# Kernel optimization log

Measured on AMD Instinct MI355X. Metric: run time of the kernel, lower is better.

## Reference

```python
import jax, jax.numpy as jnp
import numpy as np

B, L, D, H, FF = 4, 1024, 768, 12, 3072
DK = D // H
P = 32          # num_postags
MAXD = 256      # max relative distance


def _ln(x, g, b, eps):
    mu = jnp.mean(x, axis=-1, keepdims=True)
    var = jnp.mean(jnp.square(x - mu), axis=-1, keepdims=True)
    return (x - mu) * jax.lax.rsqrt(var + eps) * g + b


def setup_inputs() -> dict:
    key = jax.random.key(0)
    ks = jax.random.split(key, 16)
    s = 0.02
    return {
        "x": jax.random.normal(ks[0], (B, L, D), jnp.float32),
        "postag_ids": jax.random.randint(ks[1], (B, L), 0, P),
        "lex_mask": jax.random.normal(ks[2], (B, L), jnp.float32),
        "ln1_g": jnp.ones((D,), jnp.float32),
        "ln1_b": jnp.zeros((D,), jnp.float32),
        "Wq": jax.random.normal(ks[3], (D, D), jnp.float32) * s,
        "bq": jnp.zeros((D,), jnp.float32),
        "Wk": jax.random.normal(ks[4], (D, D), jnp.float32) * s,
        "bk": jnp.zeros((D,), jnp.float32),
        "Wv": jax.random.normal(ks[5], (D, D), jnp.float32) * s,
        "bv": jnp.zeros((D,), jnp.float32),
        "Wo": jax.random.normal(ks[6], (D, D), jnp.float32) * s,
        "bo": jnp.zeros((D,), jnp.float32),
        "rel_emb": jax.random.normal(ks[7], (2 * MAXD + 1, H), jnp.float32) * s,
        "postag_table": jax.random.normal(ks[8], (P * P, H), jnp.float32) * s,
        "ln2_g": jnp.ones((D,), jnp.float32),
        "ln2_b": jnp.zeros((D,), jnp.float32),
        "W1": jax.random.normal(ks[9], (D, FF), jnp.float32) * s,
        "b1": jnp.zeros((FF,), jnp.float32),
        "W2": jax.random.normal(ks[10], (FF, D), jnp.float32) * s,
        "b2": jnp.zeros((D,), jnp.float32),
    }


def reference(x, postag_ids, lex_mask, ln1_g, ln1_b, Wq, bq, Wk, bk, Wv, bv,
              Wo, bo, rel_emb, postag_table, ln2_g, ln2_b, W1, b1, W2, b2):
    # ---- pre-LN self-attention with rel-pos + postag + lex additive biases ----
    q_in = _ln(x, ln1_g, ln1_b, 1e-6)
    Q = (q_in @ Wq + bq).reshape(B, L, H, DK).transpose(0, 2, 1, 3)  # [B,H,L,dk]
    K = (q_in @ Wk + bk).reshape(B, L, H, DK).transpose(0, 2, 1, 3)
    V = (q_in @ Wv + bv).reshape(B, L, H, DK).transpose(0, 2, 1, 3)

    logits = jnp.einsum("bhld,bhsd->bhls", Q, K) / jnp.sqrt(jnp.float32(DK))

    # relative position bias: [H, L, L]
    idx = jnp.arange(L)
    rel = idx[None, :] - idx[:, None]
    clipped = jnp.clip(rel, -MAXD, MAXD) + MAXD
    pos_bias = rel_emb[clipped].transpose(2, 0, 1)  # [H,L,L]

    # postag pair bias: [B, H, L, L]
    pair = postag_ids[:, :, None] * P + postag_ids[:, None, :]  # [B,L,L]
    pt_bias = postag_table[pair].transpose(0, 3, 1, 2)  # [B,H,L,L]

    logits = logits + pos_bias[None] + pt_bias + lex_mask[:, None, None, :]

    attn = jax.nn.softmax(logits, axis=-1)
    out = jnp.einsum("bhls,bhsd->bhld", attn, V)
    out = out.transpose(0, 2, 1, 3).reshape(B, L, D)
    out = out @ Wo + bo + x  # residual

    # ---- FeedForward (pre-LN, exact GELU) ----
    h = _ln(out, ln2_g, ln2_b, 1e-5)
    h = jax.nn.gelu(h @ W1 + b1, approximate=False)
    return out + h @ W2 + b2
```

## Files before the change

### kernel.cpp

```cpp
#include <hip/hip_runtime.h>
#include <hip/hip_bf16.h>
#include <math.h>

typedef __hip_bfloat16 bf16;
typedef __attribute__((ext_vector_type(8))) short short8;
typedef __attribute__((ext_vector_type(4))) float f32x4;

#define BB 4
#define LL 1024
#define DD 768
#define HH 12
#define DK 64
#define FF_ 3072
#define PP 32
#define MAXD 256

__device__ __forceinline__ void async_load16(const void* g, void* l) {
    __builtin_amdgcn_global_load_lds(
        (const __attribute__((address_space(1))) unsigned int*)g,
        (__attribute__((address_space(3))) unsigned int*)l, 16, 0, 0);
}

__global__ __launch_bounds__(256) void ln_kernel(const float* __restrict__ x,
                                                 const float* __restrict__ g,
                                                 const float* __restrict__ b,
                                                 float eps,
                                                 bf16* __restrict__ y) {
    const int row = blockIdx.x;
    const int tid = threadIdx.x;
    const float* xr = x + (size_t)row * DD;

    float v[3];
    float s = 0.f, ss = 0.f;
#pragma unroll
    for (int i = 0; i < 3; ++i) {
        float t = xr[tid + i * 256];
        v[i] = t;
        s += t;
        ss += t * t;
    }
    __shared__ float rs[256], rss[256];
    rs[tid] = s; rss[tid] = ss;
    __syncthreads();
    for (int off = 128; off; off >>= 1) {
        if (tid < off) { rs[tid] += rs[tid + off]; rss[tid] += rss[tid + off]; }
        __syncthreads();
    }
    const float mean = rs[0] * (1.f / DD);
    const float var  = rss[0] * (1.f / DD) - mean * mean;
    const float inv  = rsqrtf(var + eps);
#pragma unroll
    for (int i = 0; i < 3; ++i) {
        int c = tid + i * 256;
        float o = (v[i] - mean) * inv * g[c] + b[c];
        y[(size_t)row * DD + c] = __float2bfloat16(o);
    }
}

__global__ __launch_bounds__(256) void ln_sum_kernel(const float* __restrict__ Wp,
                                                     const float* __restrict__ x,
                                                     const float* __restrict__ bo,
                                                     const float* __restrict__ g,
                                                     const float* __restrict__ b,
                                                     float eps,
                                                     float* __restrict__ out1,
                                                     bf16* __restrict__ h2) {
    const int row = blockIdx.x;
    const int tid = threadIdx.x;
    const size_t base = (size_t)row * DD;
    const size_t half = (size_t)BB * LL * DD;

    float v[3];
    float s = 0.f, ss = 0.f;
#pragma unroll
    for (int i = 0; i < 3; ++i) {
        int c = tid + i * 256;
        float t = Wp[base + c] + Wp[half + base + c] + bo[c] + x[base + c];
        out1[base + c] = t;
        v[i] = t;
        s += t;
        ss += t * t;
    }
    __shared__ float rs[256], rss[256];
    rs[tid] = s; rss[tid] = ss;
    __syncthreads();
    for (int off = 128; off; off >>= 1) {
        if (tid < off) { rs[tid] += rs[tid + off]; rss[tid] += rss[tid + off]; }
        __syncthreads();
    }
    const float mean = rs[0] * (1.f / DD);
    const float var  = rss[0] * (1.f / DD) - mean * mean;
    const float inv  = rsqrtf(var + eps);
#pragma unroll
    for (int i = 0; i < 3; ++i) {
        int c = tid + i * 256;
        float o = (v[i] - mean) * inv * g[c] + b[c];
        h2[base + c] = __float2bfloat16(o);
    }
}

__global__ __launch_bounds__(256) void ff2_reduce(const float* __restrict__ Fp,
                                                  const float* __restrict__ out1,
                                                  const float* __restrict__ b2,
                                                  float* __restrict__ dout) {
    const size_t half = (size_t)BB * LL * DD;
    const size_t i4 = (size_t)blockIdx.x * 256 + threadIdx.x;
    const size_t i = i4 * 4;
    const int c = (int)(i % DD);
    float4 p0 = *(const float4*)(Fp + i);
    float4 p1 = *(const float4*)(Fp + half + i);
    float4 r  = *(const float4*)(out1 + i);
    float4 o;
    o.x = p0.x + p1.x + r.x + b2[c];
    o.y = p0.y + p1.y + r.y + b2[c + 1];
    o.z = p0.z + p1.z + r.z + b2[c + 2];
    o.w = p0.w + p1.w + r.w + b2[c + 3];
    *(float4*)(dout + i) = o;
}

__global__ __launch_bounds__(256) void prep_weights(
        const float* __restrict__ Wq, const float* __restrict__ Wk,
        const float* __restrict__ Wv, const float* __restrict__ Wo,
        const float* __restrict__ W1, const float* __restrict__ W2,
        const float* __restrict__ bq, const float* __restrict__ bk,
        const float* __restrict__ bv,
        bf16* __restrict__ WtQKV, bf16* __restrict__ WtO,
        bf16* __restrict__ Wt1, bf16* __restrict__ Wt2,
        float* __restrict__ bqkv) {
    const int bid = blockIdx.x;
    if (bid >= 6912) {
        int i = (bid - 6912) * 256 + threadIdx.x;
        if (i < 2304) {
            float v = (i < 768) ? bq[i] : (i < 1536) ? bk[i - 768] : bv[i - 1536];
            bqkv[i] = v;
        }
        return;
    }
    const float* W; bf16* Wt; int K, N, tile;
    if (bid < 576)       { W = Wq; Wt = WtQKV;                      K = DD;  N = DD;  tile = bid; }
    else if (bid < 1152) { W = Wk; Wt = WtQKV + (size_t)768 * DD;   K = DD;  N = DD;  tile = bid - 576; }
    else if (bid < 1728) { W = Wv; Wt = WtQKV + (size_t)1536 * DD;  K = DD;  N = DD;  tile = bid - 1152; }
    else if (bid < 2304) { W = Wo; Wt = WtO;                        K = DD;  N = DD;  tile = bid - 1728; }
    else if (bid < 4608) { W = W1; Wt = Wt1;                        K = DD;  N = FF_; tile = bid - 2304; }
    else                 { W = W2; Wt = Wt2;                        K = FF_; N = DD;  tile = bid - 4608; }
    const int ntn = N / 32;
    const int n0 = (tile % ntn) * 32, k0 = (tile / ntn) * 32;

    __shared__ float tilebuf[32][33];
    const int tx = threadIdx.x & 31, ty = threadIdx.x >> 5;
#pragma unroll
    for (int i = 0; i < 4; ++i) {
        int k = ty + i * 8;
        tilebuf[k][tx] = W[(size_t)(k0 + k) * N + n0 + tx];
    }
    __syncthreads();
#pragma unroll
    for (int i = 0; i < 4; ++i) {
        int n = ty + i * 8;
        Wt[(size_t)(n0 + n) * K + k0 + tx] = __float2bfloat16(tilebuf[tx][n]);
    }
}

template <int RES, bool GELU, bool SPLIT_QKV, int KSPLIT, typename OutT>
__global__ __launch_bounds__(256) void mfma_gemm_bt(const bf16* __restrict__ A,
                                                    const bf16* __restrict__ Bt,
                                                    const float* __restrict__ bias,
                                                    const float* __restrict__ res,
                                                    OutT* __restrict__ C,
                                                    bf16* __restrict__ QhOut,
                                                    bf16* __restrict__ KhOut,
                                                    bf16* __restrict__ VtOut,
                                                    int M, int N, int K) {
    __shared__ short As[2][4096];
    __shared__ short Bs[2][4096];

    const int L = blockIdx.x + gridDim.x * (blockIdx.y + gridDim.y * blockIdx.z);
    const int xcd = L & 7, j = L >> 3;
    const int col = j % gridDim.x;
    const int panel = xcd + 8 * (j / gridDim.x);
    const int byy = panel % gridDim.y;
    const int bzz = panel / gridDim.y;

    const int bm = byy * 128, bn = col * 128;
    const int tid = threadIdx.x;
    const int w = tid >> 6, lane = tid & 63;
    const int c16 = lane & 15, quad = lane >> 4;
    const int wy = w >> 1, wx = w & 1;

    const int srow_in = lane >> 2;
    const int cg = (lane & 3) ^ quad;

    const int Ksub = K / KSPLIT;
    const int kbase = bzz * Ksub;

    f32x4 acc[4][4];
#pragma unroll
    for (int i = 0; i < 4; ++i)
#pragma unroll
        for (int j2 = 0; j2 < 4; ++j2) acc[i][j2] = (f32x4)0.f;

    auto stage = [&](int buf, int k0) {
#pragma unroll
        for (int j2 = 0; j2 < 2; ++j2) {
            const int ci = w * 2 + j2;
            const int row = ci * 16 + srow_in;
            async_load16(A + (size_t)(bm + row) * K + k0 + cg * 8, (char*)As[buf] + ci * 1024);
            async_load16(Bt + (size_t)(bn + row) * K + k0 + cg * 8, (char*)Bs[buf] + ci * 1024);
        }
    };

    const int nIter = Ksub / 32;
    stage(0, kbase);
    for (int kt = 0; kt < nIter; ++kt) {
        const int buf = kt & 1;
        __syncthreads();
        if (kt + 1 < nIter) stage(buf ^ 1, kbase + (kt + 1) * 32);

        short8 af[4], bf[4];
#pragma unroll
        for (int i = 0; i < 4; ++i) {
            const int ra = wy * 64 + i * 16 + c16;
            const int ca = quad ^ ((ra >> 2) & 3);
            af[i] = *(const short8*)((const char*)As[buf] + ra * 64 + ca * 16);
            const int rb = wx * 64 + i * 16 + c16;
            const int cb = quad ^ ((rb >> 2) & 3);
            bf[i] = *(const short8*)((const char*)Bs[buf] + rb * 64 + cb * 16);
        }
#pragma unroll
        for (int mi = 0; mi < 4; ++mi)
#pragma unroll
            for (int ni = 0; ni < 4; ++ni)
                acc[mi][ni] = __builtin_amdgcn_mfma_f32_16x16x32_bf16(af[mi], bf[ni], acc[mi][ni], 0, 0, 0);
    }

    if (KSPLIT > 1) {
        float* Cp = (float*)C + (size_t)bzz * M * N;
#pragma unroll
        for (int mi = 0; mi < 4; ++mi)
#pragma unroll
            for (int ni = 0; ni < 4; ++ni) {
                const int n = bn + wx * 64 + ni * 16 + c16;
#pragma unroll
                for (int r = 0; r < 4; ++r) {
                    const int m = bm + wy * 64 + mi * 16 + quad * 4 + r;
                    Cp[(size_t)m * N + n] = acc[mi][ni][r];
                }
            }
        return;
    }

    if (SPLIT_QKV) {
        bf16* dst; int base;
        if (bn < 768)       { dst = QhOut; base = 0; }
        else if (bn < 1536) { dst = KhOut; base = 768; }
        else                { dst = VtOut; base = 1536; }
#pragma unroll
        for (int mi = 0; mi < 4; ++mi) {
#pragma unroll
            for (int ni = 0; ni < 4; ++ni) {
                const int nfull = bn + wx * 64 + ni * 16 + c16;
                const float bv = bias[nfull];
                const int nr = nfull - base;
                const int hv = nr >> 6, dv = nr & 63;
#pragma unroll
                for (int r = 0; r < 4; ++r) {
                    const int m = bm + wy * 64 + mi * 16 + quad * 4 + r;
                    const float v = acc[mi][ni][r] + bv;
                    const size_t bh = (size_t)((m >> 10) * HH + hv);
                    if (base == 1536)
                        dst[(bh * DK + dv) * LL + (m & 1023)] = __float2bfloat16(v);
                    else
                        dst[(bh * LL + (m & 1023)) * DK + dv] = __float2bfloat16(v);
                }
            }
        }
        return;
    }

#pragma unroll
    for (int mi = 0; mi < 4; ++mi) {
#pragma unroll
        for (int ni = 0; ni < 4; ++ni) {
            const int n = bn + wx * 64 + ni * 16 + c16;
            const float bv = bias[n];
#pragma unroll
            for (int r = 0; r < 4; ++r) {
                const int m = bm + wy * 64 + mi * 16 + quad * 4 + r;
                float v = acc[mi][ni][r] + bv;
                if (GELU) v = 0.5f * v * (1.f + erff(v * 0.70710678118f));
                if (RES == 2) v += res[(size_t)m * N + n];
                if constexpr (sizeof(OutT) == 2)
                    C[(size_t)m * N + n] = __float2bfloat16(v);
                else
                    C[(size_t)m * N + n] = v;
            }
        }
    }
}

__global__ __launch_bounds__(256) void flash_attn_kernel(
        const bf16* __restrict__ Qh, const bf16* __restrict__ Kh, const bf16* __restrict__ Vt,
        const int* __restrict__ postag, const float* __restrict__ lex,
        const float* __restrict__ rel_emb, const float* __restrict__ pt_table,
        bf16* __restrict__ O) {
    const int qt = blockIdx.x;
    const int h  = blockIdx.y;
    const int b  = blockIdx.z;
    const int tid  = threadIdx.x;
    const int w    = tid >> 6;
    const int lane = tid & 63;
    const int c    = lane & 15;
    const int quad = lane >> 4;

    __shared__ short Ks[4096];
    __shared__ short Vs[4096];
    __shared__ bf16  Ps[4][16][72];
    __shared__ float rel_col[513];
    __shared__ float pt_col[1024];
    __shared__ float lex_f[LL];
    __shared__ short ps_f[LL];

    for (int i = tid; i < 513; i += 256)  rel_col[i] = rel_emb[i * HH + h];
    for (int i = tid; i < 1024; i += 256) {
        pt_col[i] = pt_table[i * HH + h];
        lex_f[i]  = lex[b * LL + i];
        ps_f[i]   = (short)postag[b * LL + i];
    }

    const int q0 = qt * 64 + w * 16;
    const size_t bh = (size_t)(b * HH + h);
    const bf16* Kbase = Kh + bh * LL * DK;
    const bf16* Vbase = Vt + bh * DK * LL;

    short8 qf0, qf1;
    {
        const bf16* qp = Qh + (bh * LL + q0 + c) * DK + quad * 8;
        qf0 = *(const short8*)qp;
        qf1 = *(const short8*)(qp + 32);
    }
    int plx_r[4];
#pragma unroll
    for (int r = 0; r < 4; ++r) plx_r[r] = postag[b * LL + q0 + quad * 4 + r] * PP;

    f32x4 o_acc[4];
#pragma unroll
    for (int t = 0; t < 4; ++t) o_acc[t] = (f32x4)0.f;
    float lsum[4] = {0.f, 0.f, 0.f, 0.f};

    const int srow = lane >> 3;
    const int schunk = lane & 7;
    __syncthreads();

    for (int s0 = 0; s0 < LL; s0 += 64) {
#pragma unroll
        for (int j = 0; j < 2; ++j) {
            const int row = w * 16 + j * 8 + srow;
            const int g = schunk ^ (row & 7);
            async_load16(Kbase + (size_t)(s0 + row) * DK + g * 8,
                         (char*)Ks + (w * 16 + j * 8) * 128);
            async_load16(Vbase + (size_t)row * LL + s0 + g * 8,
                         (char*)Vs + (w * 16 + j * 8) * 128);
        }
        __syncthreads();

        f32x4 S[4];
#pragma unroll
        for (int t = 0; t < 4; ++t) {
            const int r = t * 16 + c;
            short8 kf0 = *(const short8*)&Ks[r * 64 + ((quad ^ (r & 7)) * 8)];
            short8 kf1 = *(const short8*)&Ks[r * 64 + (((4 + quad) ^ (r & 7)) * 8)];
            f32x4 a = (f32x4)0.f;
            a = __builtin_amdgcn_mfma_f32_16x16x32_bf16(qf0, kf0, a, 0, 0, 0);
            a = __builtin_amdgcn_mfma_f32_16x16x32_bf16(qf1, kf1, a, 0, 0, 0);
            S[t] = a;
        }

        const int d0 = s0 - q0;
        if (d0 >= 271 || d0 <= -319) {
            const float rcv = rel_col[(d0 >= 271) ? 512 : 0];
#pragma unroll
            for (int t = 0; t < 4; ++t) {
                const int s_glob = s0 + t * 16 + c;
                const float lx = lex_f[s_glob] + rcv;
                const int   ps = ps_f[s_glob];
#pragma unroll
                for (int r = 0; r < 4; ++r) {
                    float e = __expf(S[t][r] * 0.125f + pt_col[plx_r[r] + ps] + lx);
                    S[t][r] = e;
                    lsum[r] += e;
                }
            }
        } else {
#pragma unroll
            for (int t = 0; t < 4; ++t) {
                const int s_glob = s0 + t * 16 + c;
                const float lx = lex_f[s_glob];
                const int   ps = ps_f[s_glob];
#pragma unroll
                for (int r = 0; r < 4; ++r) {
                    const int l_glob = q0 + quad * 4 + r;
                    const int relc = min(max(s_glob - l_glob, -MAXD), MAXD) + MAXD;
                    float e = __expf(S[t][r] * 0.125f + rel_col[relc] + pt_col[plx_r[r] + ps] + lx);
                    S[t][r] = e;
                    lsum[r] += e;
                }
            }
        }

#pragma unroll
        for (int t = 0; t < 4; ++t)
#pragma unroll
            for (int r = 0; r < 4; ++r)
                Ps[w][quad * 4 + r][t * 16 + c] = __float2bfloat16(S[t][r]);

        short8 pa0 = *(const short8*)&Ps[w][c][quad * 8];
        short8 pa1 = *(const short8*)&Ps[w][c][quad * 8 + 32];

#pragma unroll
        for (int t = 0; t < 4; ++t) {
            const int r = t * 16 + c;
            short8 vf0 = *(const short8*)&Vs[r * 64 + ((quad ^ (r & 7)) * 8)];
            short8 vf1 = *(const short8*)&Vs[r * 64 + (((4 + quad) ^ (r & 7)) * 8)];
            o_acc[t] = __builtin_amdgcn_mfma_f32_16x16x32_bf16(pa0, vf0, o_acc[t], 0, 0, 0);
            o_acc[t] = __builtin_amdgcn_mfma_f32_16x16x32_bf16(pa1, vf1, o_acc[t], 0, 0, 0);
        }
        __syncthreads();
    }

#pragma unroll
    for (int mm = 1; mm < 16; mm <<= 1)
#pragma unroll
        for (int r = 0; r < 4; ++r) lsum[r] += __shfl_xor(lsum[r], mm);

    float inv_l[4];
#pragma unroll
    for (int r = 0; r < 4; ++r) inv_l[r] = 1.f / lsum[r];
#pragma unroll
    for (int t = 0; t < 4; ++t)
#pragma unroll
        for (int r = 0; r < 4; ++r) {
            const int row = q0 + quad * 4 + r;
            O[((size_t)(b * LL + row)) * DD + h * DK + t * 16 + c] =
                __float2bfloat16(o_acc[t][r] * inv_l[r]);
        }
}

extern "C" void kernel_launch(void* const* d_in, const int* in_sizes, int n_in,
                              void* d_out, int out_size, void* d_ws, size_t ws_size,
                              hipStream_t stream) {
    const float* x          = (const float*)d_in[0];
    const int*   postag_ids = (const int*)d_in[1];
    const float* lex_mask   = (const float*)d_in[2];
    const float* ln1_g      = (const float*)d_in[3];
    const float* ln1_b      = (const float*)d_in[4];
    const float* Wq         = (const float*)d_in[5];
    const float* bq         = (const float*)d_in[6];
    const float* Wk         = (const float*)d_in[7];
    const float* bk         = (const float*)d_in[8];
    const float* Wv         = (const float*)d_in[9];
    const float* bv         = (const float*)d_in[10];
    const float* Wo         = (const float*)d_in[11];
    const float* bo         = (const float*)d_in[12];
    const float* rel_emb    = (const float*)d_in[13];
    const float* pt_table   = (const float*)d_in[14];
    const float* ln2_g      = (const float*)d_in[15];
    const float* ln2_b      = (const float*)d_in[16];
    const float* W1         = (const float*)d_in[17];
    const float* b1         = (const float*)d_in[18];
    const float* W2         = (const float*)d_in[19];
    const float* b2         = (const float*)d_in[20];

    const int M = BB * LL;
    char* ws = (char*)d_ws;
    size_t off = 0;
    bf16* y_ln  = (bf16*)(ws + off); off += (size_t)M * DD * 2;
    bf16* Qh    = (bf16*)(ws + off); off += (size_t)M * DD * 2;
    bf16* Kh    = (bf16*)(ws + off); off += (size_t)M * DD * 2;
    bf16* Vt    = (bf16*)(ws + off); off += (size_t)M * DD * 2;
    bf16* attn  = (bf16*)(ws + off); off += (size_t)M * DD * 2;
    bf16* h2    = (bf16*)(ws + off); off += (size_t)M * DD * 2;
    float* out1 = (float*)(ws + off); off += (size_t)M * DD * 4;
    bf16* ff1   = (bf16*)(ws + off); off += (size_t)M * FF_ * 2;
    bf16* WtQKV = (bf16*)(ws + off); off += (size_t)2304 * DD * 2;
    bf16* WtO   = (bf16*)(ws + off); off += (size_t)DD * DD * 2;
    bf16* Wt1   = (bf16*)(ws + off); off += (size_t)FF_ * DD * 2;
    bf16* Wt2   = (bf16*)(ws + off); off += (size_t)DD * FF_ * 2;
    float* bqkv = (float*)(ws + off); off += (size_t)2304 * 4;
    float* Part = (float*)ws;

    prep_weights<<<6921, 256, 0, stream>>>(Wq, Wk, Wv, Wo, W1, W2, bq, bk, bv,
                                           WtQKV, WtO, Wt1, Wt2, bqkv);

    ln_kernel<<<M, 256, 0, stream>>>(x, ln1_g, ln1_b, 1e-6f, y_ln);

    mfma_gemm_bt<0, false, true, 1, bf16><<<dim3(2304 / 128, M / 128), 256, 0, stream>>>(
        y_ln, WtQKV, bqkv, nullptr, (bf16*)nullptr, Qh, Kh, Vt, M, 2304, DD);

    flash_attn_kernel<<<dim3(LL / 64, HH, BB), 256, 0, stream>>>(
        Qh, Kh, Vt, postag_ids, lex_mask, rel_emb, pt_table, attn);

    mfma_gemm_bt<0, false, false, 2, float><<<dim3(DD / 128, M / 128, 2), 256, 0, stream>>>(
        attn, WtO, nullptr, nullptr, Part, nullptr, nullptr, nullptr, M, DD, DD);

    ln_sum_kernel<<<M, 256, 0, stream>>>(Part, x, bo, ln2_g, ln2_b, 1e-5f, out1, h2);

    mfma_gemm_bt<0, true, false, 1, bf16><<<dim3(FF_ / 128, M / 128), 256, 0, stream>>>(
        h2, Wt1, b1, nullptr, ff1, nullptr, nullptr, nullptr, M, FF_, DD);

    mfma_gemm_bt<0, false, false, 2, float><<<dim3(DD / 128, M / 128, 2), 256, 0, stream>>>(
        ff1, Wt2, nullptr, nullptr, Part, nullptr, nullptr, nullptr, M, DD, FF_);

    ff2_reduce<<<(M * DD / 4) / 256, 256, 0, stream>>>(Part, out1, b2, (float*)d_out);
}
```

Before: 306.8 us.

## Merge LN1 into weight prep, split FF2 four ways with bf16 partials, vectorize rel-bias

Result: faster. 293.3 us (-4.4%).

```diff
diff --git a/kernel.cpp b/kernel.cpp
--- a/kernel.cpp
+++ b/kernel.cpp
@@ -21,39 +21,78 @@
         (__attribute__((address_space(3))) unsigned int*)l, 16, 0, 0);
 }
 
-__global__ __launch_bounds__(256) void ln_kernel(const float* __restrict__ x,
-                                                 const float* __restrict__ g,
-                                                 const float* __restrict__ b,
-                                                 float eps,
-                                                 bf16* __restrict__ y) {
-    const int row = blockIdx.x;
+__global__ __launch_bounds__(256) void prep_ln(
+        const float* __restrict__ x,
+        const float* __restrict__ ln1_g, const float* __restrict__ ln1_b,
+        const float* __restrict__ Wq, const float* __restrict__ Wk,
+        const float* __restrict__ Wv, const float* __restrict__ Wo,
+        const float* __restrict__ W1, const float* __restrict__ W2,
+        const float* __restrict__ bq, const float* __restrict__ bk,
+        const float* __restrict__ bv,
+        bf16* __restrict__ y_ln,
+        bf16* __restrict__ WtQKV, bf16* __restrict__ WtO,
+        bf16* __restrict__ Wt1, bf16* __restrict__ Wt2,
+        float* __restrict__ bqkv) {
+    const int bid = blockIdx.x;
     const int tid = threadIdx.x;
-    const float* xr = x + (size_t)row * DD;
-
-    float v[3];
-    float s = 0.f, ss = 0.f;
-#pragma unroll
-    for (int i = 0; i < 3; ++i) {
-        float t = xr[tid + i * 256];
-        v[i] = t;
-        s += t;
-        ss += t * t;
-    }
-    __shared__ float rs[256], rss[256];
-    rs[tid] = s; rss[tid] = ss;
+
+    if (bid < 4096) {
+        const float* xr = x + (size_t)bid * DD;
+        float v[3];
+        float s = 0.f, ss = 0.f;
+#pragma unroll
+        for (int i = 0; i < 3; ++i) {
+            float t = xr[tid + i * 256];
+            v[i] = t; s += t; ss += t * t;
+        }
+        __shared__ float rs[256], rss[256];
+        rs[tid] = s; rss[tid] = ss;
+        __syncthreads();
+        for (int off = 128; off; off >>= 1) {
+            if (tid < off) { rs[tid] += rs[tid + off]; rss[tid] += rss[tid + off]; }
+            __syncthreads();
+        }
+        const float mean = rs[0] * (1.f / DD);
+        const float var  = rss[0] * (1.f / DD) - mean * mean;
+        const float inv  = rsqrtf(var + 1e-6f);
+#pragma unroll
+        for (int i = 0; i < 3; ++i) {
+            int c = tid + i * 256;
+            y_ln[(size_t)bid * DD + c] = __float2bfloat16((v[i] - mean) * inv * ln1_g[c] + ln1_b[c]);
+        }
+        return;
+    }
+    if (bid >= 11008) {
+        int i = (bid - 11008) * 256 + tid;
+        if (i < 2304) {
+            float v = (i < 768) ? bq[i] : (i < 1536) ? bk[i - 768] : bv[i - 1536];
+            bqkv[i] = v;
+        }
+        return;
+    }
+    const int tb = bid - 4096;
+    const float* W; bf16* Wt; int K, N, tile;
+    if (tb < 576)       { W = Wq; Wt = WtQKV;                      K = DD;  N = DD;  tile = tb; }
+    else if (tb < 1152) { W = Wk; Wt = WtQKV + (size_t)768 * DD;   K = DD;  N = DD;  tile = tb - 576; }
+    else if (tb < 1728) { W = Wv; Wt = WtQKV + (size_t)1536 * DD;  K = DD;  N = DD;  tile = tb - 1152; }
+    else if (tb < 2304) { W = Wo; Wt = WtO;                        K = DD;  N = DD;  tile = tb - 1728; }
+    else if (tb < 4608) { W = W1; Wt = Wt1;                        K = DD;  N = FF_; tile = tb - 2304; }
+    else                { W = W2; Wt = Wt2;                        K = FF_; N = DD;  tile = tb - 4608; }
+    const int ntn = N / 32;
+    const int n0 = (tile % ntn) * 32, k0 = (tile / ntn) * 32;
+
+    __shared__ float tilebuf[32][33];
+    const int tx = tid & 31, ty = tid >> 5;
+#pragma unroll
+    for (int i = 0; i < 4; ++i) {
+        int k = ty + i * 8;
+        tilebuf[k][tx] = W[(size_t)(k0 + k) * N + n0 + tx];
+    }
     __syncthreads();
-    for (int off = 128; off; off >>= 1) {
-        if (tid < off) { rs[tid] += rs[tid + off]; rss[tid] += rss[tid + off]; }
-        __syncthreads();
-    }
-    const float mean = rs[0] * (1.f / DD);
-    const float var  = rss[0] * (1.f / DD) - mean * mean;
-    const float inv  = rsqrtf(var + eps);
-#pragma unroll
-    for (int i = 0; i < 3; ++i) {
-        int c = tid + i * 256;
-        float o = (v[i] - mean) * inv * g[c] + b[c];
-        y[(size_t)row * DD + c] = __float2bfloat16(o);
+#pragma unroll
+    for (int i = 0; i < 4; ++i) {
+        int n = ty + i * 8;
+        Wt[(size_t)(n0 + n) * K + k0 + tx] = __float2bfloat16(tilebuf[tx][n]);
     }
 }
 
@@ -77,9 +116,7 @@
         int c = tid + i * 256;
         float t = Wp[base + c] + Wp[half + base + c] + bo[c] + x[base + c];
         out1[base + c] = t;
-        v[i] = t;
-        s += t;
-        ss += t * t;
+        v[i] = t; s += t; ss += t * t;
     }
     __shared__ float rs[256], rss[256];
     rs[tid] = s; rss[tid] = ss;
@@ -94,71 +131,35 @@
 #pragma unroll
     for (int i = 0; i < 3; ++i) {
         int c = tid + i * 256;
-        float o = (v[i] - mean) * inv * g[c] + b[c];
-        h2[base + c] = __float2bfloat16(o);
-    }
-}
-
-__global__ __launch_bounds__(256) void ff2_reduce(const float* __restrict__ Fp,
+        h2[base + c] = __float2bfloat16((v[i] - mean) * inv * g[c] + b[c]);
+    }
+}
+
+__global__ __launch_bounds__(256) void ff2_reduce(const bf16* __restrict__ Fp,
                                                   const float* __restrict__ out1,
                                                   const float* __restrict__ b2,
                                                   float* __restrict__ dout) {
-    const size_t half = (size_t)BB * LL * DD;
-    const size_t i4 = (size_t)blockIdx.x * 256 + threadIdx.x;
-    const size_t i = i4 * 4;
-    const int c = (int)(i % DD);
-    float4 p0 = *(const float4*)(Fp + i);
-    float4 p1 = *(const float4*)(Fp + half + i);
-    float4 r  = *(const float4*)(out1 + i);
-    float4 o;
-    o.x = p0.x + p1.x + r.x + b2[c];
-    o.y = p0.y + p1.y + r.y + b2[c + 1];
-    o.z = p0.z + p1.z + r.z + b2[c + 2];
-    o.w = p0.w + p1.w + r.w + b2[c + 3];
-    *(float4*)(dout + i) = o;
-}
-
-__global__ __launch_bounds__(256) void prep_weights(
-        const float* __restrict__ Wq, const float* __restrict__ Wk,
-        const float* __restrict__ Wv, const float* __restrict__ Wo,
-        const float* __restrict__ W1, const float* __restrict__ W2,
-        const float* __restrict__ bq, const float* __restrict__ bk,
-        const float* __restrict__ bv,
-        bf16* __restrict__ WtQKV, bf16* __restrict__ WtO,
-        bf16* __restrict__ Wt1, bf16* __restrict__ Wt2,
-        float* __restrict__ bqkv) {
-    const int bid = blockIdx.x;
-    if (bid >= 6912) {
-        int i = (bid - 6912) * 256 + threadIdx.x;
-        if (i < 2304) {
-            float v = (i < 768) ? bq[i] : (i < 1536) ? bk[i - 768] : bv[i - 1536];
-            bqkv[i] = v;
-        }
-        return;
-    }
-    const float* W; bf16* Wt; int K, N, tile;
-    if (bid < 576)       { W = Wq; Wt = WtQKV;                      K = DD;  N = DD;  tile = bid; }
-    else if (bid < 1152) { W = Wk; Wt = WtQKV + (size_t)768 * DD;   K = DD;  N = DD;  tile = bid - 576; }
-    else if (bid < 1728) { W = Wv; Wt = WtQKV + (size_t)1536 * DD;  K = DD;  N = DD;  tile = bid - 1152; }
-    else if (bid < 2304) { W = Wo; Wt = WtO;                        K = DD;  N = DD;  tile = bid - 1728; }
-    else if (bid < 4608) { W = W1; Wt = Wt1;                        K = DD;  N = FF_; tile = bid - 2304; }
-    else                 { W = W2; Wt = Wt2;                        K = FF_; N = DD;  tile = bid - 4608; }
-    const int ntn = N / 32;
-    const int n0 = (tile % ntn) * 32, k0 = (tile / ntn) * 32;
-
-    __shared__ float tilebuf[32][33];
-    const int tx = threadIdx.x & 31, ty = threadIdx.x >> 5;
-#pragma unroll
-    for (int i = 0; i < 4; ++i) {
-        int k = ty + i * 8;
-        tilebuf[k][tx] = W[(size_t)(k0 + k) * N + n0 + tx];
-    }
-    __syncthreads();
-#pragma unroll
-    for (int i = 0; i < 4; ++i) {
-        int n = ty + i * 8;
-        Wt[(size_t)(n0 + n) * K + k0 + tx] = __float2bfloat16(tilebuf[tx][n]);
-    }
+    const size_t stride = (size_t)BB * LL * DD;
+    const size_t i8 = ((size_t)blockIdx.x * 256 + threadIdx.x) * 8;
+    const int c = (int)(i8 % DD);
+
+    float acc[8];
+    float4 r0 = *(const float4*)(out1 + i8);
+    float4 r1 = *(const float4*)(out1 + i8 + 4);
+    float4 bb0 = *(const float4*)(b2 + c);
+    float4 bb1 = *(const float4*)(b2 + c + 4);
+    acc[0] = r0.x + bb0.x; acc[1] = r0.y + bb0.y; acc[2] = r0.z + bb0.z; acc[3] = r0.w + bb0.w;
+    acc[4] = r1.x + bb1.x; acc[5] = r1.y + bb1.y; acc[6] = r1.z + bb1.z; acc[7] = r1.w + bb1.w;
+#pragma unroll
+    for (int p = 0; p < 4; ++p) {
+        short8 v = *(const short8*)(Fp + p * stride + i8);
+#pragma unroll
+        for (int k = 0; k < 8; ++k) acc[k] += __bfloat162float(((const bf16*)&v)[k]);
+    }
+    float4 o0 = {acc[0], acc[1], acc[2], acc[3]};
+    float4 o1 = {acc[4], acc[5], acc[6], acc[7]};
+    *(float4*)(dout + i8) = o0;
+    *(float4*)(dout + i8 + 4) = o1;
 }
 
 template <int RES, bool GELU, bool SPLIT_QKV, int KSPLIT, typename OutT>
@@ -234,7 +235,7 @@
     }
 
     if (KSPLIT > 1) {
-        float* Cp = (float*)C + (size_t)bzz * M * N;
+        OutT* Cp = C + (size_t)bzz * M * N;
 #pragma unroll
         for (int mi = 0; mi < 4; ++mi)
 #pragma unroll
@@ -243,7 +244,10 @@
 #pragma unroll
                 for (int r = 0; r < 4; ++r) {
                     const int m = bm + wy * 64 + mi * 16 + quad * 4 + r;
-                    Cp[(size_t)m * N + n] = acc[mi][ni][r];
+                    if constexpr (sizeof(OutT) == 2)
+                        Cp[(size_t)m * N + n] = __float2bfloat16(acc[mi][ni][r]);
+                    else
+                        Cp[(size_t)m * N + n] = acc[mi][ni][r];
                 }
             }
         return;
@@ -315,12 +319,19 @@
     __shared__ short Ks[4096];
     __shared__ short Vs[4096];
     __shared__ bf16  Ps[4][16][72];
-    __shared__ float rel_col[513];
+    __shared__ f32x4 relT[516];
     __shared__ float pt_col[1024];
     __shared__ float lex_f[LL];
     __shared__ short ps_f[LL];
 
-    for (int i = tid; i < 513; i += 256)  rel_col[i] = rel_emb[i * HH + h];
+    for (int i = tid; i < 516; i += 256) {
+        f32x4 t;
+        t[0] = rel_emb[min(i, 512) * HH + h];
+        t[1] = rel_emb[min(max(i - 1, 0), 512) * HH + h];
+        t[2] = rel_emb[min(max(i - 2, 0), 512) * HH + h];
+        t[3] = rel_emb[min(max(i - 3, 0), 512) * HH + h];
+        relT[i] = t;
+    }
     for (int i = tid; i < 1024; i += 256) {
         pt_col[i] = pt_table[i * HH + h];
         lex_f[i]  = lex[b * LL + i];
@@ -377,7 +388,7 @@
 
         const int d0 = s0 - q0;
         if (d0 >= 271 || d0 <= -319) {
-            const float rcv = rel_col[(d0 >= 271) ? 512 : 0];
+            const float rcv = (d0 >= 271) ? relT[515][0] : relT[0][0];
 #pragma unroll
             for (int t = 0; t < 4; ++t) {
                 const int s_glob = s0 + t * 16 + c;
@@ -391,18 +402,20 @@
                 }
             }
         } else {
+            const int ebase = d0 - quad * 4 + 256;
 #pragma unroll
             for (int t = 0; t < 4; ++t) {
-                const int s_glob = s0 + t * 16 + c;
+                const int s_loc = t * 16 + c;
+                const int s_glob = s0 + s_loc;
                 const float lx = lex_f[s_glob];
                 const int   ps = ps_f[s_glob];
+                const int e = min(max(ebase + s_loc, 0), 515);
+                f32x4 rv = relT[e];
 #pragma unroll
                 for (int r = 0; r < 4; ++r) {
-                    const int l_glob = q0 + quad * 4 + r;
-                    const int relc = min(max(s_glob - l_glob, -MAXD), MAXD) + MAXD;
-                    float e = __expf(S[t][r] * 0.125f + rel_col[relc] + pt_col[plx_r[r] + ps] + lx);
-                    S[t][r] = e;
-                    lsum[r] += e;
+                    float ev = __expf(S[t][r] * 0.125f + rv[r] + pt_col[plx_r[r] + ps] + lx);
+                    S[t][r] = ev;
+                    lsum[r] += ev;
                 }
             }
         }
@@ -486,12 +499,11 @@
     bf16* Wt1   = (bf16*)(ws + off); off += (size_t)FF_ * DD * 2;
     bf16* Wt2   = (bf16*)(ws + off); off += (size_t)DD * FF_ * 2;
     float* bqkv = (float*)(ws + off); off += (size_t)2304 * 4;
-    float* Part = (float*)ws;
-
-    prep_weights<<<6921, 256, 0, stream>>>(Wq, Wk, Wv, Wo, W1, W2, bq, bk, bv,
-                                           WtQKV, WtO, Wt1, Wt2, bqkv);
-
-    ln_kernel<<<M, 256, 0, stream>>>(x, ln1_g, ln1_b, 1e-6f, y_ln);
+    float* PartWo = (float*)ws;
+    bf16*  PartF2 = (bf16*)ws;
+
+    prep_ln<<<11017, 256, 0, stream>>>(x, ln1_g, ln1_b, Wq, Wk, Wv, Wo, W1, W2,
+                                       bq, bk, bv, y_ln, WtQKV, WtO, Wt1, Wt2, bqkv);
 
     mfma_gemm_bt<0, false, true, 1, bf16><<<dim3(2304 / 128, M / 128), 256, 0, stream>>>(
         y_ln, WtQKV, bqkv, nullptr, (bf16*)nullptr, Qh, Kh, Vt, M, 2304, DD);
@@ -500,15 +512,15 @@
         Qh, Kh, Vt, postag_ids, lex_mask, rel_emb, pt_table, attn);
 
     mfma_gemm_bt<0, false, false, 2, float><<<dim3(DD / 128, M / 128, 2), 256, 0, stream>>>(
-        attn, WtO, nullptr, nullptr, Part, nullptr, nullptr, nullptr, M, DD, DD);
-
-    ln_sum_kernel<<<M, 256, 0, stream>>>(Part, x, bo, ln2_g, ln2_b, 1e-5f, out1, h2);
+        attn, WtO, nullptr, nullptr, PartWo, nullptr, nullptr, nullptr, M, DD, DD);
+
+    ln_sum_kernel<<<M, 256, 0, stream>>>(PartWo, x, bo, ln2_g, ln2_b, 1e-5f, out1, h2);
 
     mfma_gemm_bt<0, true, false, 1, bf16><<<dim3(FF_ / 128, M / 128), 256, 0, stream>>>(
         h2, Wt1, b1, nullptr, ff1, nullptr, nullptr, nullptr, M, FF_, DD);
 
-    mfma_gemm_bt<0, false, false, 2, float><<<dim3(DD / 128, M / 128, 2), 256, 0, stream>>>(
-        ff1, Wt2, nullptr, nullptr, Part, nullptr, nullptr, nullptr, M, DD, FF_);
-
-    ff2_reduce<<<(M * DD / 4) / 256, 256, 0, stream>>>(Part, out1, b2, (float*)d_out);
-}
+    mfma_gemm_bt<0, false, false, 4, bf16><<<dim3(DD / 128, M / 128, 4), 256, 0, stream>>>(
+        ff1, Wt2, nullptr, nullptr, PartF2, nullptr, nullptr, nullptr, M, DD, FF_);
+
+    ff2_reduce<<<(M * DD / 8) / 256, 256, 0, stream>>>(PartF2, out1, b2, (float*)d_out);
+}
```
